# Optimization experiments

Measured on AMD Instinct MI355X. Metric: run time of the kernel, lower is better.

Reference implementation:

```python
import jax, jax.numpy as jnp
import numpy as np

N_NODES = 100000
N_EDGES = 1600000
D = 128  # 2 * config.out_channels with config.out_channels = 64


def setup_inputs() -> dict:
    key = jax.random.key(0)
    k1, k2, k3, k4 = jax.random.split(key, 4)
    x_in = jax.random.normal(k1, (N_NODES, D), dtype=jnp.float32)
    x_out = jax.random.normal(k2, (N_NODES, D), dtype=jnp.float32)
    edge_index = jax.random.randint(k3, (2, N_EDGES), 0, N_NODES, dtype=jnp.int64)
    # nn.Bilinear(D, D, 1, bias=False) weight: [out_features=1, D, D]
    W = jax.random.normal(k4, (1, D, D), dtype=jnp.float32) * (1.0 / np.sqrt(D))
    return {"x_in": x_in, "x_out": x_out, "edge_index": edge_index, "W": W}


def reference(x_in, x_out, edge_index, W):
    # Gather edge endpoint features (irregular access)
    a = x_out[edge_index[0]]          # [E, D]
    b = x_in[edge_index[1]]           # [E, D]
    # Bilinear form with single output: value_e = a_e^T W0 b_e
    W0 = W[0]                         # [D, D]
    aW = a @ W0                       # [E, D]
    value = jnp.sum(aW * b, axis=-1)  # [E]
    return jax.nn.sigmoid(value)
```

## Files before the change

### kernel.cpp

```cpp
#include <hip/hip_runtime.h>
#include <hip/hip_fp16.h>
#include <math.h>

#define D 128
#define GM 64
#define CONV_BLOCKS 2048
#define CONV_BLOCKS_OLD 1024

typedef _Float16 f16x8 __attribute__((ext_vector_type(8)));
typedef float    f32x4 __attribute__((ext_vector_type(4)));
typedef _Float16 h2_t  __attribute__((ext_vector_type(2)));

__device__ __forceinline__ float dot2acc(unsigned ua, unsigned ub, float c) {
#if __has_builtin(__builtin_amdgcn_fdot2)
  return __builtin_amdgcn_fdot2(__builtin_bit_cast(h2_t, ua),
                                __builtin_bit_cast(h2_t, ub), c, false);
#else
  __half2 a = __builtin_bit_cast(__half2, ua);
  __half2 b = __builtin_bit_cast(__half2, ub);
  float2 fa = __half22float2(a), fb = __half22float2(b);
  return fmaf(fa.x, fb.x, fmaf(fa.y, fb.y, c));
#endif
}

__device__ __forceinline__ unsigned pack2(float x, float y) {
  __half2 h;
  h.x = __float2half_rn(x);
  h.y = __float2half_rn(y);
  return __builtin_bit_cast(unsigned, h);
}

__global__ __launch_bounds__(256) void wt_kernel(const float* __restrict__ W,
                                                 __half* __restrict__ WhT) {
  const int n  = blockIdx.x * 16 + (threadIdx.x >> 4);
  const int k0 = (threadIdx.x & 15) * 8;
  float w[8];
  #pragma unroll
  for (int kk = 0; kk < 8; kk++) w[kk] = W[(k0 + kk) * D + n];
  uint4 u;
  u.x = pack2(w[0], w[1]); u.y = pack2(w[2], w[3]);
  u.z = pack2(w[4], w[5]); u.w = pack2(w[6], w[7]);
  *(uint4*)(WhT + n * D + k0) = u;
}

__global__ __launch_bounds__(256) void prep2_kernel(
    const float* __restrict__ Xout, const float* __restrict__ Xin,
    const __half* __restrict__ WhT, __half* __restrict__ Yh,
    __half* __restrict__ Xh, int N, int gemm_blocks)
{
  __shared__ __align__(16) __half sA[GM * D];

  const int tid = threadIdx.x;

  if ((int)blockIdx.x >= gemm_blocks) {
    const int cb = blockIdx.x - gemm_blocks;
    const int n4 = N * (D / 4);
    const int stride = CONV_BLOCKS * 256 * 4;
    for (int base = (cb * 256 + tid) * 4; base < n4; base += stride) {
      float4 v[4];
      #pragma unroll
      for (int j = 0; j < 4; j++)
        if (base + j < n4) v[j] = ((const float4*)Xin)[base + j];
      #pragma unroll
      for (int j = 0; j < 4; j++)
        if (base + j < n4) {
          uint2 u;
          u.x = pack2(v[j].x, v[j].y);
          u.y = pack2(v[j].z, v[j].w);
          ((uint2*)Xh)[base + j] = u;
        }
    }
    return;
  }

  const int row0 = blockIdx.x * GM;

  float4 v[8];
  #pragma unroll
  for (int i = 0; i < 4; i++) {
    int gi = tid + i * 256;
    int r = gi >> 4, q = gi & 15;
    int gr = row0 + r;
    if (gr < N) {
      const float4* s = (const float4*)(Xout + (size_t)gr * D + q * 8);
      v[2*i]   = s[0];
      v[2*i+1] = s[1];
    } else {
      v[2*i]   = make_float4(0.f, 0.f, 0.f, 0.f);
      v[2*i+1] = make_float4(0.f, 0.f, 0.f, 0.f);
    }
  }
  #pragma unroll
  for (int i = 0; i < 4; i++) {
    int gi = tid + i * 256;
    int r = gi >> 4, q = gi & 15;
    uint4 u;
    u.x = pack2(v[2*i].x,   v[2*i].y);
    u.y = pack2(v[2*i].z,   v[2*i].w);
    u.z = pack2(v[2*i+1].x, v[2*i+1].y);
    u.w = pack2(v[2*i+1].z, v[2*i+1].w);
    *(uint4*)(sA + r * D + ((q ^ (r & 7)) << 3)) = u;
  }
  __syncthreads();

  const int lane = tid & 63, wave = tid >> 6;
  const int m = lane & 15, quad = lane >> 4;
  const int rloc = wave * 16 + m;

  f32x4 acc[8];
  #pragma unroll
  for (int ct = 0; ct < 8; ct++) acc[ct] = (f32x4){0.f, 0.f, 0.f, 0.f};

  #pragma unroll
  for (int ks = 0; ks < 4; ks++) {
    const int g = ks * 4 + quad;
    f16x8 bfrag[8];
    #pragma unroll
    for (int ct = 0; ct < 8; ct++)
      bfrag[ct] = *(const f16x8*)(WhT + (size_t)(ct * 16 + m) * D + g * 8);
    f16x8 afrag = *(const f16x8*)(sA + rloc * D + ((g ^ (rloc & 7)) << 3));
    #pragma unroll
    for (int ct = 0; ct < 8; ct++)
      acc[ct] = __builtin_amdgcn_mfma_f32_16x16x32_f16(
          afrag, bfrag[ct], acc[ct], 0, 0, 0);
  }

  __syncthreads();
  __half* sC = sA;
  #pragma unroll
  for (int ct = 0; ct < 8; ct++)
    #pragma unroll
    for (int reg = 0; reg < 4; reg++) {
      int r = wave * 16 + quad * 4 + reg;
      sC[r * D + ct * 16 + m] = __float2half_rn(acc[ct][reg]);
    }
  __syncthreads();
  #pragma unroll
  for (int i = 0; i < 4; i++) {
    int gi = tid + i * 256;
    int r = gi >> 4, q = gi & 15;
    int gr = row0 + r;
    if (gr < N)
      *(uint4*)(Yh + (size_t)gr * D + q * 8) = *(const uint4*)(sC + r * D + q * 8);
  }
}

__global__ __launch_bounds__(256) void prep_kernel(
    const float* __restrict__ Xout, const float* __restrict__ Xin,
    const float* __restrict__ W, __half* __restrict__ Yh,
    __half* __restrict__ Xh, int N, int gemm_blocks)
{
  __shared__ __align__(16) __half sA[128 * 128];
  __shared__ __align__(16) __half sB[128 * 128];

  const int tid = threadIdx.x;

  if ((int)blockIdx.x >= gemm_blocks) {
    const int cb = blockIdx.x - gemm_blocks;
    const int n4 = N * (D / 4);
    const int stride = CONV_BLOCKS_OLD * 256 * 4;
    for (int base = (cb * 256 + tid) * 4; base < n4; base += stride) {
      float4 v[4];
      #pragma unroll
      for (int j = 0; j < 4; j++)
        if (base + j < n4) v[j] = ((const float4*)Xin)[base + j];
      #pragma unroll
      for (int j = 0; j < 4; j++)
        if (base + j < n4) {
          uint2 u;
          u.x = pack2(v[j].x, v[j].y);
          u.y = pack2(v[j].z, v[j].w);
          ((uint2*)Xh)[base + j] = u;
        }
    }
    return;
  }

  const int row0 = blockIdx.x * 128;

  #pragma unroll
  for (int i = 0; i < 16; i++) {
    int idx = tid + i * 256;
    int q   = idx & 31;
    int r   = idx >> 5;
    int gr  = row0 + r;
    float4 v = make_float4(0.f, 0.f, 0.f, 0.f);
    if (gr < N) v = *(const float4*)(Xout + (size_t)gr * D + q * 4);
    uint2 u;
    u.x = pack2(v.x, v.y);
    u.y = pack2(v.z, v.w);
    int g   = q >> 1;
    int sub = q & 1;
    int off = r * 128 + (((g + r) & 15) << 3) + (sub << 2);
    *(uint2*)(sA + off) = u;
  }
  #pragma unroll
  for (int i = 0; i < 64; i++) {
    int o = tid + i * 256;
    int k = o >> 7;
    int n = o & 127;
    __half h = __float2half_rn(W[o]);
    int gk = k >> 3;
    sB[n * 128 + (((gk + n) & 15) << 3) + (k & 7)] = h;
  }
  __syncthreads();

  const int wave = tid >> 6;
  const int lane = tid & 63;
  const int m    = lane & 15;
  const int quad = lane >> 4;

  f32x4 acc[2][8];
  #pragma unroll
  for (int rt = 0; rt < 2; rt++)
    #pragma unroll
    for (int ct = 0; ct < 8; ct++)
      acc[rt][ct] = (f32x4){0.f, 0.f, 0.f, 0.f};

  #pragma unroll
  for (int ks = 0; ks < 4; ks++) {
    const int g = ks * 4 + quad;
    f16x8 bfrag[8];
    #pragma unroll
    for (int ct = 0; ct < 8; ct++) {
      int n = ct * 16 + m;
      bfrag[ct] = *(const f16x8*)(sB + n * 128 + (((g + n) & 15) << 3));
    }
    #pragma unroll
    for (int rt = 0; rt < 2; rt++) {
      int r = wave * 32 + rt * 16 + m;
      f16x8 afrag = *(const f16x8*)(sA + r * 128 + (((g + r) & 15) << 3));
      #pragma unroll
      for (int ct = 0; ct < 8; ct++)
        acc[rt][ct] = __builtin_amdgcn_mfma_f32_16x16x32_f16(
            afrag, bfrag[ct], acc[rt][ct], 0, 0, 0);
    }
  }

  __syncthreads();
  __half* sC = sA;
  #pragma unroll
  for (int rt = 0; rt < 2; rt++)
    #pragma unroll
    for (int reg = 0; reg < 4; reg++) {
      int r = wave * 32 + rt * 16 + quad * 4 + reg;
      #pragma unroll
      for (int ct = 0; ct < 8; ct++)
        sC[r * 128 + ct * 16 + m] = __float2half_rn(acc[rt][ct][reg]);
    }
  __syncthreads();
  #pragma unroll
  for (int i = 0; i < 8; i++) {
    int idx = tid + i * 256;
    int r   = idx >> 4;
    int gq  = idx & 15;
    int gr  = row0 + r;
    if (gr < N)
      *(uint4*)(Yh + (size_t)gr * D + gq * 8) = *(const uint4*)(sC + r * 128 + gq * 8);
  }
}

__global__ __launch_bounds__(256) void edge_dot4_kernel(
    const __half* __restrict__ Yh, const __half* __restrict__ Xh,
    const int* __restrict__ idx, float* __restrict__ out, int E)
{
  long long gid = (long long)blockIdx.x * 256 + threadIdx.x;
  int slot = (int)(gid >> 4);
  int l    = (int)(gid & 15);
  int e0 = slot * 4;
  if (e0 >= E) return;

  int s[4], d[4];
  #pragma unroll
  for (int i = 0; i < 4; i++) {
    int e = e0 + i; if (e > E - 1) e = E - 1;
    s[i] = idx[e];
    d[i] = idx[E + e];
  }
  uint4 a[4], b[4];
  #pragma unroll
  for (int i = 0; i < 4; i++) a[i] = ((const uint4*)(Yh + (size_t)s[i] * D))[l];
  #pragma unroll
  for (int i = 0; i < 4; i++) b[i] = ((const uint4*)(Xh + (size_t)d[i] * D))[l];

  float p[4];
  #pragma unroll
  for (int i = 0; i < 4; i++) {
    float t = 0.f;
    t = dot2acc(a[i].x, b[i].x, t);
    t = dot2acc(a[i].y, b[i].y, t);
    t = dot2acc(a[i].z, b[i].z, t);
    t = dot2acc(a[i].w, b[i].w, t);
    p[i] = t;
  }
  #pragma unroll
  for (int i = 0; i < 4; i++) {
    p[i] += __shfl_xor(p[i], 8);
    p[i] += __shfl_xor(p[i], 4);
    p[i] += __shfl_xor(p[i], 2);
    p[i] += __shfl_xor(p[i], 1);
  }

  if (l == 0) {
    float4 o;
    o.x = 1.0f / (1.0f + __expf(-p[0]));
    o.y = 1.0f / (1.0f + __expf(-p[1]));
    o.z = 1.0f / (1.0f + __expf(-p[2]));
    o.w = 1.0f / (1.0f + __expf(-p[3]));
    if (e0 + 3 < E) {
      *(float4*)(out + e0) = o;
    } else {
      out[e0] = o.x;
      if (e0 + 1 < E) out[e0 + 1] = o.y;
      if (e0 + 2 < E) out[e0 + 2] = o.z;
    }
  }
}

__global__ __launch_bounds__(256) void edge_bilinear_direct_kernel(
    const float* __restrict__ Xout, const float* __restrict__ Xin,
    const float* __restrict__ W, const int* __restrict__ idx,
    float* __restrict__ out, int E)
{
  long long gid = (long long)blockIdx.x * 256 + threadIdx.x;
  int e = (int)(gid >> 6);
  if (e >= E) return;
  int l = (int)(gid & 63);

  int src = idx[e];
  int dst = idx[E + e];
  const float* a = Xout + (size_t)src * D;
  const float* b = Xin  + (size_t)dst * D;

  float s = 0.f;
  #pragma unroll
  for (int kk = 0; kk < 2; kk++) {
    int k = l + kk * 64;
    float ak = a[k];
    float t = 0.f;
    #pragma unroll 8
    for (int j = 0; j < D; j++) t = fmaf(W[(size_t)k * D + j], b[j], t);
    s = fmaf(ak, t, s);
  }
  #pragma unroll
  for (int off = 32; off >= 1; off >>= 1) s += __shfl_xor(s, off);
  if (l == 0) out[e] = 1.0f / (1.0f + __expf(-s));
}

extern "C" void kernel_launch(void* const* d_in, const int* in_sizes, int n_in,
                              void* d_out, int out_size, void* d_ws, size_t ws_size,
                              hipStream_t stream) {
  const float* x_in  = (const float*)d_in[0];
  const float* x_out = (const float*)d_in[1];
  const int*   eidx  = (const int*)d_in[2];
  const float* W     = (const float*)d_in[3];
  float* out = (float*)d_out;

  const int N = in_sizes[0] / D;
  const int E = in_sizes[2] / 2;

  const size_t half_rows = (size_t)N * D * sizeof(__half);
  const size_t wht_bytes = (size_t)D * D * sizeof(__half);

  if (ws_size >= 2 * half_rows + wht_bytes) {
    __half* Yh  = (__half*)d_ws;
    __half* Xh  = (__half*)((char*)d_ws + half_rows);
    __half* WhT = (__half*)((char*)d_ws + 2 * half_rows);

    wt_kernel<<<dim3(8), 256, 0, stream>>>(W, WhT);

    int gemm_blocks = (N + GM - 1) / GM;
    dim3 g1(gemm_blocks + CONV_BLOCKS);
    prep2_kernel<<<g1, 256, 0, stream>>>(x_out, x_in, WhT, Yh, Xh, N, gemm_blocks);

    long long slots = ((long long)E + 3) / 4;
    long long total = slots * 16;
    dim3 g2((unsigned)((total + 255) / 256));
    edge_dot4_kernel<<<g2, 256, 0, stream>>>(Yh, Xh, eidx, out, E);
  } else if (ws_size >= 2 * half_rows) {
    __half* Yh = (__half*)d_ws;
    __half* Xh = (__half*)((char*)d_ws + half_rows);

    int gemm_blocks = (N + 127) / 128;
    dim3 g1(gemm_blocks + CONV_BLOCKS_OLD);
    prep_kernel<<<g1, 256, 0, stream>>>(x_out, x_in, W, Yh, Xh, N, gemm_blocks);

    long long slots = ((long long)E + 3) / 4;
    long long total = slots * 16;
    dim3 g2((unsigned)((total + 255) / 256));
    edge_dot4_kernel<<<g2, 256, 0, stream>>>(Yh, Xh, eidx, out, E);
  } else {
    long long total = (long long)E * 64;
    dim3 g((unsigned)((total + 255) / 256));
    edge_bilinear_direct_kernel<<<g, 256, 0, stream>>>(x_out, x_in, W, eidx, out, E);
  }
}
```

Measured before the change: 261.9 us.

## Bucket-sort edges by source node to improve gather locality

Adds a counting-sort pipeline (histogram, scan, and an atomic scatter fused into the prep kernel) that groups edges by source-node bucket. The edge kernel then reads sorted (src,dst) pairs, so Yh row gathers are more cache-local, and remaps workgroups across XCDs so each XCD gets a contiguous range. Outputs are scattered back through the original edge ids. In exchange it adds extra passes over the edge indices, global atomics, extra workspace, and scattered 4-byte output writes.

```diff
diff --git a/kernel.cpp b/kernel.cpp
--- a/kernel.cpp
+++ b/kernel.cpp
@@ -5,7 +5,11 @@
 #define D 128
 #define GM 64
 #define CONV_BLOCKS 2048
+#define SCAT_BLOCKS 1024
+#define HIST_BLOCKS 1024
 #define CONV_BLOCKS_OLD 1024
+#define NBSHIFT 6
+#define NBINS 2048
 
 typedef _Float16 f16x8 __attribute__((ext_vector_type(8)));
 typedef float    f32x4 __attribute__((ext_vector_type(4)));
@@ -30,17 +34,215 @@
   return __builtin_bit_cast(unsigned, h);
 }
 
-__global__ __launch_bounds__(256) void wt_kernel(const float* __restrict__ W,
-                                                 __half* __restrict__ WhT) {
-  const int n  = blockIdx.x * 16 + (threadIdx.x >> 4);
-  const int k0 = (threadIdx.x & 15) * 8;
-  float w[8];
-  #pragma unroll
-  for (int kk = 0; kk < 8; kk++) w[kk] = W[(k0 + kk) * D + n];
-  uint4 u;
-  u.x = pack2(w[0], w[1]); u.y = pack2(w[2], w[3]);
-  u.z = pack2(w[4], w[5]); u.w = pack2(w[6], w[7]);
-  *(uint4*)(WhT + n * D + k0) = u;
+__global__ __launch_bounds__(256) void setup_kernel(const float* __restrict__ W,
+                                                    __half* __restrict__ WhT,
+                                                    int* __restrict__ cnt) {
+  if ((int)blockIdx.x < 8) {
+    const int n  = blockIdx.x * 16 + (threadIdx.x >> 4);
+    const int k0 = (threadIdx.x & 15) * 8;
+    float w[8];
+    #pragma unroll
+    for (int kk = 0; kk < 8; kk++) w[kk] = W[(k0 + kk) * D + n];
+    uint4 u;
+    u.x = pack2(w[0], w[1]); u.y = pack2(w[2], w[3]);
+    u.z = pack2(w[4], w[5]); u.w = pack2(w[6], w[7]);
+    *(uint4*)(WhT + n * D + k0) = u;
+  } else {
+    for (int i = threadIdx.x; i < NBINS; i += 256) cnt[i] = 0;
+  }
+}
+
+__global__ __launch_bounds__(256) void hist_kernel(const int* __restrict__ eidx,
+                                                   int* __restrict__ cnt, int E) {
+  for (int e = blockIdx.x * 256 + threadIdx.x; e < E; e += HIST_BLOCKS * 256)
+    atomicAdd(&cnt[eidx[e] >> NBSHIFT], 1);
+}
+
+__global__ __launch_bounds__(256) void scan_kernel(const int* __restrict__ cnt,
+                                                   int* __restrict__ cursor) {
+  __shared__ int tsum[256];
+  const int tid = threadIdx.x;
+  int v[NBINS / 256];
+  int s = 0;
+  #pragma unroll
+  for (int j = 0; j < NBINS / 256; j++) {
+    v[j] = cnt[tid * (NBINS / 256) + j];
+    s += v[j];
+  }
+  tsum[tid] = s;
+  __syncthreads();
+  for (int off = 1; off < 256; off <<= 1) {
+    int t = (tid >= off) ? tsum[tid - off] : 0;
+    __syncthreads();
+    tsum[tid] += t;
+    __syncthreads();
+  }
+  int ex = (tid > 0) ? tsum[tid - 1] : 0;
+  #pragma unroll
+  for (int j = 0; j < NBINS / 256; j++) {
+    cursor[tid * (NBINS / 256) + j] = ex;
+    ex += v[j];
+  }
+}
+
+__global__ __launch_bounds__(256) void fused_kernel(
+    const float* __restrict__ Xout, const float* __restrict__ Xin,
+    const __half* __restrict__ WhT, __half* __restrict__ Yh,
+    __half* __restrict__ Xh, const int* __restrict__ eidx,
+    int2* __restrict__ sortedSD, int* __restrict__ sortedE,
+    int* __restrict__ cursor, int N, int E, int gemm_blocks)
+{
+  __shared__ __align__(16) __half sA[GM * D];
+
+  const int tid = threadIdx.x;
+  const int bid = blockIdx.x;
+
+  if (bid >= gemm_blocks + CONV_BLOCKS) {
+    const int sb = bid - gemm_blocks - CONV_BLOCKS;
+    for (int e = sb * 256 + tid; e < E; e += SCAT_BLOCKS * 256) {
+      int s = eidx[e];
+      int d = eidx[E + e];
+      int pos = atomicAdd(&cursor[s >> NBSHIFT], 1);
+      sortedSD[pos] = make_int2(s, d);
+      sortedE[pos]  = e;
+    }
+    return;
+  }
+
+  if (bid >= gemm_blocks) {
+    const int cb = bid - gemm_blocks;
+    const int n4 = N * (D / 4);
+    const int stride = CONV_BLOCKS * 256 * 4;
+    for (int base = (cb * 256 + tid) * 4; base < n4; base += stride) {
+      float4 v[4];
+      #pragma unroll
+      for (int j = 0; j < 4; j++)
+        if (base + j < n4) v[j] = ((const float4*)Xin)[base + j];
+      #pragma unroll
+      for (int j = 0; j < 4; j++)
+        if (base + j < n4) {
+          uint2 u;
+          u.x = pack2(v[j].x, v[j].y);
+          u.y = pack2(v[j].z, v[j].w);
+          ((uint2*)Xh)[base + j] = u;
+        }
+    }
+    return;
+  }
+
+  const int row0 = bid * GM;
+
+  float4 v[8];
+  #pragma unroll
+  for (int i = 0; i < 4; i++) {
+    int gi = tid + i * 256;
+    int r = gi >> 4, q = gi & 15;
+    int gr = row0 + r;
+    if (gr < N) {
+      const float4* s = (const float4*)(Xout + (size_t)gr * D + q * 8);
+      v[2*i]   = s[0];
+      v[2*i+1] = s[1];
+    } else {
+      v[2*i]   = make_float4(0.f, 0.f, 0.f, 0.f);
+      v[2*i+1] = make_float4(0.f, 0.f, 0.f, 0.f);
+    }
+  }
+  #pragma unroll
+  for (int i = 0; i < 4; i++) {
+    int gi = tid + i * 256;
+    int r = gi >> 4, q = gi & 15;
+    uint4 u;
+    u.x = pack2(v[2*i].x,   v[2*i].y);
+    u.y = pack2(v[2*i].z,   v[2*i].w);
+    u.z = pack2(v[2*i+1].x, v[2*i+1].y);
+    u.w = pack2(v[2*i+1].z, v[2*i+1].w);
+    *(uint4*)(sA + r * D + ((q ^ (r & 7)) << 3)) = u;
+  }
+  __syncthreads();
+
+  const int lane = tid & 63, wave = tid >> 6;
+  const int m = lane & 15, quad = lane >> 4;
+  const int rloc = wave * 16 + m;
+
+  f32x4 acc[8];
+  #pragma unroll
+  for (int ct = 0; ct < 8; ct++) acc[ct] = (f32x4){0.f, 0.f, 0.f, 0.f};
+
+  #pragma unroll
+  for (int ks = 0; ks < 4; ks++) {
+    const int g = ks * 4 + quad;
+    f16x8 bfrag[8];
+    #pragma unroll
+    for (int ct = 0; ct < 8; ct++)
+      bfrag[ct] = *(const f16x8*)(WhT + (size_t)(ct * 16 + m) * D + g * 8);
+    f16x8 afrag = *(const f16x8*)(sA + rloc * D + ((g ^ (rloc & 7)) << 3));
+    #pragma unroll
+    for (int ct = 0; ct < 8; ct++)
+      acc[ct] = __builtin_amdgcn_mfma_f32_16x16x32_f16(
+          afrag, bfrag[ct], acc[ct], 0, 0, 0);
+  }
+
+  __syncthreads();
+  __half* sC = sA;
+  #pragma unroll
+  for (int ct = 0; ct < 8; ct++)
+    #pragma unroll
+    for (int reg = 0; reg < 4; reg++) {
+      int r = wave * 16 + quad * 4 + reg;
+      sC[r * D + ct * 16 + m] = __float2half_rn(acc[ct][reg]);
+    }
+  __syncthreads();
+  #pragma unroll
+  for (int i = 0; i < 4; i++) {
+    int gi = tid + i * 256;
+    int r = gi >> 4, q = gi & 15;
+    int gr = row0 + r;
+    if (gr < N)
+      *(uint4*)(Yh + (size_t)gr * D + q * 8) = *(const uint4*)(sC + r * D + q * 8);
+  }
+}
+
+__global__ __launch_bounds__(256) void edge_sorted_kernel(
+    const __half* __restrict__ Yh, const __half* __restrict__ Xh,
+    const int2* __restrict__ sortedSD, const int* __restrict__ sortedE,
+    float* __restrict__ out, int E)
+{
+  const int nwg = gridDim.x, orig = blockIdx.x;
+  const int xcd = orig & 7, rest = orig >> 3;
+  const int q8 = nwg >> 3, r8 = nwg & 7;
+  const int wg = (xcd < r8) ? (xcd * (q8 + 1) + rest)
+                            : (r8 * (q8 + 1) + (xcd - r8) * q8 + rest);
+
+  long long gid = (long long)wg * 256 + threadIdx.x;
+  int grp = (int)(gid >> 4);
+  int l   = (int)(gid & 15);
+  int e0 = grp * 2;
+  if (e0 >= E) return;
+  bool has1 = (e0 + 1 < E);
+
+  int2 sd0 = sortedSD[e0];
+  int2 sd1 = has1 ? sortedSD[e0 + 1] : sd0;
+
+  uint4 a0 = ((const uint4*)(Yh + (size_t)sd0.x * D))[l];
+  uint4 b0 = ((const uint4*)(Xh + (size_t)sd0.y * D))[l];
+  uint4 a1 = ((const uint4*)(Yh + (size_t)sd1.x * D))[l];
+  uint4 b1 = ((const uint4*)(Xh + (size_t)sd1.y * D))[l];
+
+  float p = 0.f, qd = 0.f;
+  p = dot2acc(a0.x, b0.x, p);  qd = dot2acc(a1.x, b1.x, qd);
+  p = dot2acc(a0.y, b0.y, p);  qd = dot2acc(a1.y, b1.y, qd);
+  p = dot2acc(a0.z, b0.z, p);  qd = dot2acc(a1.z, b1.z, qd);
+  p = dot2acc(a0.w, b0.w, p);  qd = dot2acc(a1.w, b1.w, qd);
+
+  p  += __shfl_xor(p, 8);   qd += __shfl_xor(qd, 8);
+  p  += __shfl_xor(p, 4);   qd += __shfl_xor(qd, 4);
+  p  += __shfl_xor(p, 2);   qd += __shfl_xor(qd, 2);
+  p  += __shfl_xor(p, 1);   qd += __shfl_xor(qd, 1);
+
+  if (l == 0) {
+    out[sortedE[e0]] = 1.0f / (1.0f + __expf(-p));
+    if (has1) out[sortedE[e0 + 1]] = 1.0f / (1.0f + __expf(-qd));
+  }
 }
 
 __global__ __launch_bounds__(256) void prep2_kernel(
@@ -145,175 +347,45 @@
   }
 }
 
-__global__ __launch_bounds__(256) void prep_kernel(
-    const float* __restrict__ Xout, const float* __restrict__ Xin,
-    const float* __restrict__ W, __half* __restrict__ Yh,
-    __half* __restrict__ Xh, int N, int gemm_blocks)
-{
-  __shared__ __align__(16) __half sA[128 * 128];
-  __shared__ __align__(16) __half sB[128 * 128];
-
-  const int tid = threadIdx.x;
-
-  if ((int)blockIdx.x >= gemm_blocks) {
-    const int cb = blockIdx.x - gemm_blocks;
-    const int n4 = N * (D / 4);
-    const int stride = CONV_BLOCKS_OLD * 256 * 4;
-    for (int base = (cb * 256 + tid) * 4; base < n4; base += stride) {
-      float4 v[4];
-      #pragma unroll
-      for (int j = 0; j < 4; j++)
-        if (base + j < n4) v[j] = ((const float4*)Xin)[base + j];
-      #pragma unroll
-      for (int j = 0; j < 4; j++)
-        if (base + j < n4) {
-          uint2 u;
-          u.x = pack2(v[j].x, v[j].y);
-          u.y = pack2(v[j].z, v[j].w);
-          ((uint2*)Xh)[base + j] = u;
-        }
-    }
-    return;
-  }
-
-  const int row0 = blockIdx.x * 128;
-
-  #pragma unroll
-  for (int i = 0; i < 16; i++) {
-    int idx = tid + i * 256;
-    int q   = idx & 31;
-    int r   = idx >> 5;
-    int gr  = row0 + r;
-    float4 v = make_float4(0.f, 0.f, 0.f, 0.f);
-    if (gr < N) v = *(const float4*)(Xout + (size_t)gr * D + q * 4);
-    uint2 u;
-    u.x = pack2(v.x, v.y);
-    u.y = pack2(v.z, v.w);
-    int g   = q >> 1;
-    int sub = q & 1;
-    int off = r * 128 + (((g + r) & 15) << 3) + (sub << 2);
-    *(uint2*)(sA + off) = u;
-  }
-  #pragma unroll
-  for (int i = 0; i < 64; i++) {
-    int o = tid + i * 256;
-    int k = o >> 7;
-    int n = o & 127;
-    __half h = __float2half_rn(W[o]);
-    int gk = k >> 3;
-    sB[n * 128 + (((gk + n) & 15) << 3) + (k & 7)] = h;
-  }
-  __syncthreads();
-
-  const int wave = tid >> 6;
-  const int lane = tid & 63;
-  const int m    = lane & 15;
-  const int quad = lane >> 4;
-
-  f32x4 acc[2][8];
-  #pragma unroll
-  for (int rt = 0; rt < 2; rt++)
-    #pragma unroll
-    for (int ct = 0; ct < 8; ct++)
-      acc[rt][ct] = (f32x4){0.f, 0.f, 0.f, 0.f};
-
-  #pragma unroll
-  for (int ks = 0; ks < 4; ks++) {
-    const int g = ks * 4 + quad;
-    f16x8 bfrag[8];
-    #pragma unroll
-    for (int ct = 0; ct < 8; ct++) {
-      int n = ct * 16 + m;
-      bfrag[ct] = *(const f16x8*)(sB + n * 128 + (((g + n) & 15) << 3));
-    }
-    #pragma unroll
-    for (int rt = 0; rt < 2; rt++) {
-      int r = wave * 32 + rt * 16 + m;
-      f16x8 afrag = *(const f16x8*)(sA + r * 128 + (((g + r) & 15) << 3));
-      #pragma unroll
-      for (int ct = 0; ct < 8; ct++)
-        acc[rt][ct] = __builtin_amdgcn_mfma_f32_16x16x32_f16(
-            afrag, bfrag[ct], acc[rt][ct], 0, 0, 0);
-    }
-  }
-
-  __syncthreads();
-  __half* sC = sA;
-  #pragma unroll
-  for (int rt = 0; rt < 2; rt++)
-    #pragma unroll
-    for (int reg = 0; reg < 4; reg++) {
-      int r = wave * 32 + rt * 16 + quad * 4 + reg;
-      #pragma unroll
-      for (int ct = 0; ct < 8; ct++)
-        sC[r * 128 + ct * 16 + m] = __float2half_rn(acc[rt][ct][reg]);
-    }
-  __syncthreads();
-  #pragma unroll
-  for (int i = 0; i < 8; i++) {
-    int idx = tid + i * 256;
-    int r   = idx >> 4;
-    int gq  = idx & 15;
-    int gr  = row0 + r;
-    if (gr < N)
-      *(uint4*)(Yh + (size_t)gr * D + gq * 8) = *(const uint4*)(sC + r * 128 + gq * 8);
-  }
-}
-
-__global__ __launch_bounds__(256) void edge_dot4_kernel(
+__global__ __launch_bounds__(256) void edge_dot2_kernel(
     const __half* __restrict__ Yh, const __half* __restrict__ Xh,
     const int* __restrict__ idx, float* __restrict__ out, int E)
 {
   long long gid = (long long)blockIdx.x * 256 + threadIdx.x;
   int slot = (int)(gid >> 4);
   int l    = (int)(gid & 15);
-  int e0 = slot * 4;
+  int e0 = slot * 2;
   if (e0 >= E) return;
-
-  int s[4], d[4];
-  #pragma unroll
-  for (int i = 0; i < 4; i++) {
-    int e = e0 + i; if (e > E - 1) e = E - 1;
-    s[i] = idx[e];
-    d[i] = idx[E + e];
-  }
-  uint4 a[4], b[4];
-  #pragma unroll
-  for (int i = 0; i < 4; i++) a[i] = ((const uint4*)(Yh + (size_t)s[i] * D))[l];
-  #pragma unroll
-  for (int i = 0; i < 4; i++) b[i] = ((const uint4*)(Xh + (size_t)d[i] * D))[l];
-
-  float p[4];
-  #pragma unroll
-  for (int i = 0; i < 4; i++) {
-    float t = 0.f;
-    t = dot2acc(a[i].x, b[i].x, t);
-    t = dot2acc(a[i].y, b[i].y, t);
-    t = dot2acc(a[i].z, b[i].z, t);
-    t = dot2acc(a[i].w, b[i].w, t);
-    p[i] = t;
-  }
-  #pragma unroll
-  for (int i = 0; i < 4; i++) {
-    p[i] += __shfl_xor(p[i], 8);
-    p[i] += __shfl_xor(p[i], 4);
-    p[i] += __shfl_xor(p[i], 2);
-    p[i] += __shfl_xor(p[i], 1);
-  }
+  int e1 = e0 + 1;
+  bool has1 = (e1 < E);
+
+  int s0 = idx[e0];
+  int d0 = idx[E + e0];
+  int s1 = has1 ? idx[e1] : s0;
+  int d1 = has1 ? idx[E + e1] : d0;
+
+  uint4 a0 = ((const uint4*)(Yh + (size_t)s0 * D))[l];
+  uint4 b0 = ((const uint4*)(Xh + (size_t)d0 * D))[l];
+  uint4 a1 = ((const uint4*)(Yh + (size_t)s1 * D))[l];
+  uint4 b1 = ((const uint4*)(Xh + (size_t)d1 * D))[l];
+
+  float p = 0.f, q = 0.f;
+  p = dot2acc(a0.x, b0.x, p);  q = dot2acc(a1.x, b1.x, q);
+  p = dot2acc(a0.y, b0.y, p);  q = dot2acc(a1.y, b1.y, q);
+  p = dot2acc(a0.z, b0.z, p);  q = dot2acc(a1.z, b1.z, q);
+  p = dot2acc(a0.w, b0.w, p);  q = dot2acc(a1.w, b1.w, q);
+
+  p += __shfl_xor(p, 8);  q += __shfl_xor(q, 8);
+  p += __shfl_xor(p, 4);  q += __shfl_xor(q, 4);
+  p += __shfl_xor(p, 2);  q += __shfl_xor(q, 2);
+  p += __shfl_xor(p, 1);  q += __shfl_xor(q, 1);
 
   if (l == 0) {
-    float4 o;
-    o.x = 1.0f / (1.0f + __expf(-p[0]));
-    o.y = 1.0f / (1.0f + __expf(-p[1]));
-    o.z = 1.0f / (1.0f + __expf(-p[2]));
-    o.w = 1.0f / (1.0f + __expf(-p[3]));
-    if (e0 + 3 < E) {
-      *(float4*)(out + e0) = o;
-    } else {
-      out[e0] = o.x;
-      if (e0 + 1 < E) out[e0 + 1] = o.y;
-      if (e0 + 2 < E) out[e0 + 2] = o.z;
-    }
+    float2 o;
+    o.x = 1.0f / (1.0f + __expf(-p));
+    o.y = 1.0f / (1.0f + __expf(-q));
+    if (has1) *(float2*)(out + e0) = o;
+    else      out[e0] = o.x;
   }
 }
 
@@ -361,34 +433,55 @@
 
   const size_t half_rows = (size_t)N * D * sizeof(__half);
   const size_t wht_bytes = (size_t)D * D * sizeof(__half);
-
-  if (ws_size >= 2 * half_rows + wht_bytes) {
+  const size_t cnt_bytes = (size_t)NBINS * sizeof(int);
+  const size_t sd_bytes  = (size_t)E * sizeof(int2);
+  const size_t se_bytes  = (size_t)E * sizeof(int);
+
+  size_t off_yh  = 0;
+  size_t off_xh  = off_yh + half_rows;
+  size_t off_wht = off_xh + half_rows;
+  size_t off_cnt = off_wht + wht_bytes;
+  size_t off_cur = off_cnt + cnt_bytes;
+  size_t off_sd  = off_cur + cnt_bytes;
+  size_t off_se  = off_sd + sd_bytes;
+  size_t total_ws = off_se + se_bytes;
+
+  if (ws_size >= total_ws && N <= (NBINS << NBSHIFT)) {
+    __half* Yh   = (__half*)((char*)d_ws + off_yh);
+    __half* Xh   = (__half*)((char*)d_ws + off_xh);
+    __half* WhT  = (__half*)((char*)d_ws + off_wht);
+    int*  cnt    = (int*)((char*)d_ws + off_cnt);
+    int*  cursor = (int*)((char*)d_ws + off_cur);
+    int2* sSD    = (int2*)((char*)d_ws + off_sd);
+    int*  sE     = (int*)((char*)d_ws + off_se);
+
+    setup_kernel<<<dim3(9), 256, 0, stream>>>(W, WhT, cnt);
+    hist_kernel<<<dim3(HIST_BLOCKS), 256, 0, stream>>>(eidx, cnt, E);
+    scan_kernel<<<dim3(1), 256, 0, stream>>>(cnt, cursor);
+
+    int gemm_blocks = (N + GM - 1) / GM;
+    dim3 gd(gemm_blocks + CONV_BLOCKS + SCAT_BLOCKS);
+    fused_kernel<<<gd, 256, 0, stream>>>(x_out, x_in, WhT, Yh, Xh, eidx,
+                                         sSD, sE, cursor, N, E, gemm_blocks);
+
+    long long groups = ((long long)E + 1) / 2;
+    unsigned eblocks = (unsigned)((groups * 16 + 255) / 256);
+    edge_sorted_kernel<<<dim3(eblocks), 256, 0, stream>>>(Yh, Xh, sSD, sE, out, E);
+  } else if (ws_size >= 2 * half_rows + wht_bytes) {
     __half* Yh  = (__half*)d_ws;
     __half* Xh  = (__half*)((char*)d_ws + half_rows);
     __half* WhT = (__half*)((char*)d_ws + 2 * half_rows);
 
-    wt_kernel<<<dim3(8), 256, 0, stream>>>(W, WhT);
+    setup_kernel<<<dim3(8), 256, 0, stream>>>(W, WhT, (int*)WhT );
 
     int gemm_blocks = (N + GM - 1) / GM;
     dim3 g1(gemm_blocks + CONV_BLOCKS);
     prep2_kernel<<<g1, 256, 0, stream>>>(x_out, x_in, WhT, Yh, Xh, N, gemm_blocks);
 
-    long long slots = ((long long)E + 3) / 4;
+    long long slots = ((long long)E + 1) / 2;
     long long total = slots * 16;
     dim3 g2((unsigned)((total + 255) / 256));
-    edge_dot4_kernel<<<g2, 256, 0, stream>>>(Yh, Xh, eidx, out, E);
-  } else if (ws_size >= 2 * half_rows) {
-    __half* Yh = (__half*)d_ws;
-    __half* Xh = (__half*)((char*)d_ws + half_rows);
-
-    int gemm_blocks = (N + 127) / 128;
-    dim3 g1(gemm_blocks + CONV_BLOCKS_OLD);
-    prep_kernel<<<g1, 256, 0, stream>>>(x_out, x_in, W, Yh, Xh, N, gemm_blocks);
-
-    long long slots = ((long long)E + 3) / 4;
-    long long total = slots * 16;
-    dim3 g2((unsigned)((total + 255) / 256));
-    edge_dot4_kernel<<<g2, 256, 0, stream>>>(Yh, Xh, eidx, out, E);
+    edge_dot2_kernel<<<g2, 256, 0, stream>>>(Yh, Xh, eidx, out, E);
   } else {
     long long total = (long long)E * 64;
     dim3 g((unsigned)((total + 255) / 256));
```

Measured after the change: 704.6 us. 2.69x slower.
